# Kernel optimization log

Measured on AMD Instinct MI355X. Metric: run time of the kernel, lower is better.

## Reference

```python
import jax, jax.numpy as jnp
import numpy as np

NORM_EPS = 1e-6


def setup_inputs() -> dict:
    key = jax.random.key(0)
    k1, k2 = jax.random.split(key)
    in_features, out_features = 4096, 4096
    x = jax.random.normal(k1, (2, 2048, in_features), dtype=jnp.float32)
    scale = 1.0 / np.sqrt(in_features)
    weight = jax.random.normal(k2, (out_features, in_features), dtype=jnp.float32) * scale
    norm_weight = jnp.ones((in_features,), dtype=jnp.float32)
    return {"x": x, "weight": weight, "norm_weight": norm_weight}


def reference(x, weight, norm_weight):
    # RMSNorm over the last dim
    rms = jnp.sqrt(jnp.mean(x * x, axis=-1, keepdims=True) + NORM_EPS)
    x_n = x / rms * norm_weight
    # ternary weight quantization (absmean scale alpha)
    alpha = jnp.maximum(jnp.mean(jnp.abs(weight)), 1e-10)
    w_q = jnp.clip(jnp.round(weight / alpha), -1.0, 1.0)
    # per-token int8 activation quantization (absmax scale gamma)
    gamma = jnp.maximum(jnp.max(jnp.abs(x_n), axis=-1, keepdims=True), 1e-10)
    x_q = jnp.clip(jnp.round(x_n * 127.0 / gamma), -128.0, 127.0)
    # rescaled matmul: y = x_q @ w_q.T * (alpha * gamma / 127)
    y = jnp.einsum('bsk,nk->bsn', x_q, w_q) * (alpha * gamma / 127.0)
    return y
```

## Files before the change

### kernel.cpp

```cpp
#include <hip/hip_runtime.h>
#include <cstdint>
#include <cstddef>


#define KD 4096
#define MD 4096
#define ND 4096

#define WBLK 512

typedef int i32x4 __attribute__((ext_vector_type(4)));

__device__ __forceinline__ void gl2lds16(const signed char* g, signed char* l) {
  __builtin_amdgcn_global_load_lds(
      (const __attribute__((address_space(1))) void*)g,
      (__attribute__((address_space(3))) void*)l, 16, 0, 0);
}

__device__ __forceinline__ float wave_sum(float v) {
#pragma unroll
  for (int off = 32; off; off >>= 1) v += __shfl_down(v, off, 64);
  return v;
}
__device__ __forceinline__ float wave_max(float v) {
#pragma unroll
  for (int off = 32; off; off >>= 1) v = fmaxf(v, __shfl_down(v, off, 64));
  return v;
}


__global__ __launch_bounds__(256) void k_alpha_part(const float* __restrict__ w,
                                                    float* __restrict__ part) {
  __shared__ float red[4];
  const int tid = threadIdx.x;
  const float4* w4 = (const float4*)(w + (size_t)blockIdx.x * 4096);
  float s = 0.f;
#pragma unroll
  for (int i = 0; i < 4; ++i) {
    float4 v = w4[i * 256 + tid];
    s += fabsf(v.x) + fabsf(v.y) + fabsf(v.z) + fabsf(v.w);
  }
  s = wave_sum(s);
  if ((tid & 63) == 0) red[tid >> 6] = s;
  __syncthreads();
  if (tid == 0) part[blockIdx.x] = (red[0] + red[1]) + (red[2] + red[3]);
}


__device__ __forceinline__ uint32_t qw4(float4 v, float alpha) {
  int q0 = (int)fminf(fmaxf(rintf(v.x / alpha), -1.f), 1.f);
  int q1 = (int)fminf(fmaxf(rintf(v.y / alpha), -1.f), 1.f);
  int q2 = (int)fminf(fmaxf(rintf(v.z / alpha), -1.f), 1.f);
  int q3 = (int)fminf(fmaxf(rintf(v.w / alpha), -1.f), 1.f);
  return (uint32_t)(q0 & 255) | ((uint32_t)(q1 & 255) << 8) |
         ((uint32_t)(q2 & 255) << 16) | ((uint32_t)(q3 & 255) << 24);
}

__global__ __launch_bounds__(256) void k_quant_all(const float* __restrict__ w,
                                                   const float* __restrict__ x,
                                                   const float* __restrict__ nw,
                                                   const float* __restrict__ part,
                                                   signed char* __restrict__ wq,
                                                   signed char* __restrict__ xq,
                                                   float* __restrict__ gamma,
                                                   float* __restrict__ alpha_out) {
  const int tid = threadIdx.x;
  const int bid = blockIdx.x;
  __shared__ float red[4];
  __shared__ float red2[4];

  if (bid < 4096) {
    const int row = bid;
    const float4* x4 = (const float4*)(x + (size_t)row * 4096);
    const float4* n4 = (const float4*)nw;
    float4 xv[4], nv[4];
#pragma unroll
    for (int i = 0; i < 4; ++i) {
      xv[i] = x4[i * 256 + tid];
      nv[i] = n4[i * 256 + tid];
    }
    float ss = 0.f, mx = 0.f;
#pragma unroll
    for (int i = 0; i < 4; ++i) {
      ss += xv[i].x * xv[i].x + xv[i].y * xv[i].y + xv[i].z * xv[i].z +
            xv[i].w * xv[i].w;
      mx = fmaxf(mx,
                 fmaxf(fmaxf(fabsf(xv[i].x * nv[i].x), fabsf(xv[i].y * nv[i].y)),
                       fmaxf(fabsf(xv[i].z * nv[i].z), fabsf(xv[i].w * nv[i].w))));
    }
    ss = wave_sum(ss);
    mx = wave_max(mx);
    if ((tid & 63) == 0) {
      red[tid >> 6] = ss;
      red2[tid >> 6] = mx;
    }
    __syncthreads();
    const float tot = (red[0] + red[1]) + (red[2] + red[3]);
    const float rms = sqrtf(tot * (1.0f / 4096.0f) + 1e-6f);
    const float mxr = fmaxf(fmaxf(red2[0], red2[1]), fmaxf(red2[2], red2[3]));
    const float g = fmaxf(mxr / rms, 1e-10f);
    if (tid == 0) gamma[row] = g;
    const float inv = 127.0f / (rms * g);

    uint32_t* xqi = (uint32_t*)(xq + (size_t)row * 4096);
#pragma unroll
    for (int i = 0; i < 4; ++i) {
      const int f = i * 256 + tid;
      int q0 = (int)fminf(fmaxf(rintf(xv[i].x * nv[i].x * inv), -128.f), 127.f);
      int q1 = (int)fminf(fmaxf(rintf(xv[i].y * nv[i].y * inv), -128.f), 127.f);
      int q2 = (int)fminf(fmaxf(rintf(xv[i].z * nv[i].z * inv), -128.f), 127.f);
      int q3 = (int)fminf(fmaxf(rintf(xv[i].w * nv[i].w * inv), -128.f), 127.f);
      xqi[f] = (uint32_t)(q0 & 255) | ((uint32_t)(q1 & 255) << 8) |
               ((uint32_t)(q2 & 255) << 16) | ((uint32_t)(q3 & 255) << 24);
    }
  } else {
    const int wb = bid - 4096;
    float s = 0.f;
#pragma unroll
    for (int i = 0; i < 16; ++i) s += part[i * 256 + tid];
    s = wave_sum(s);
    if ((tid & 63) == 0) red[tid >> 6] = s;
    __syncthreads();
    const float alpha =
        fmaxf(((red[0] + red[1]) + (red[2] + red[3])) * (1.0f / 16777216.0f),
              1e-10f);
    if (wb == 0 && tid == 0) alpha_out[0] = alpha;

    const float4* w4 = (const float4*)w;
    uint32_t* wqi = (uint32_t*)wq;
#pragma unroll 1
    for (int k = 0; k < 32; k += 4) {
      const int f0 = (wb * 32 + k) * 256 + tid;
      float4 v0 = w4[f0];
      float4 v1 = w4[f0 + 256];
      float4 v2 = w4[f0 + 512];
      float4 v3 = w4[f0 + 768];
      wqi[f0] = qw4(v0, alpha);
      wqi[f0 + 256] = qw4(v1, alpha);
      wqi[f0 + 512] = qw4(v2, alpha);
      wqi[f0 + 768] = qw4(v3, alpha);
    }
  }
}


#define BM 256
#define BN 256
#define BK 64

__global__ __launch_bounds__(512, 2) void k_gemm(const signed char* __restrict__ xq,
                                                 const signed char* __restrict__ wq,
                                                 const float* __restrict__ gamma,
                                                 const float* __restrict__ alpha_p,
                                                 float* __restrict__ out) {
  __shared__ __align__(16) signed char As_[2 * 16384];
  const int tid = threadIdx.x;
  const int lane = tid & 63;
  const int wave = tid >> 6;
  const int wm = (wave >> 2) * 128;
  const int wn = (wave & 3) * 64;
  const int quad = lane >> 4;
  const int l16 = lane & 15;

  const int x = blockIdx.x & 7;
  const int r = blockIdx.x >> 3;
  const int bm = ((x & 3) * 4 + (r >> 3)) * BM;
  const int bn = ((x >> 2) * 8 + (r & 7)) * BN;

  const int lr = lane >> 2;
  const int sc = (lane & 3) ^ ((lane >> 3) & 3);
  const int rb0 = wave * 16;
  const int rb1 = (8 + wave) * 16;
  const signed char* ag0 = xq + (size_t)(bm + rb0 + lr) * KD + sc * 16;
  const signed char* ag1 = xq + (size_t)(bm + rb1 + lr) * KD + sc * 16;
  const int lA0 = rb0 * BK;
  const int lA1 = rb1 * BK;

  const int pos = (quad ^ ((l16 >> 1) & 3)) * 16;

  const signed char* bgf[4];
#pragma unroll
  for (int ni = 0; ni < 4; ++ni)
    bgf[ni] = wq + (size_t)(bn + wn + ni * 16 + l16) * KD + quad * 16;

  i32x4 acc[8][4];
#pragma unroll
  for (int i = 0; i < 8; ++i)
#pragma unroll
    for (int j = 0; j < 4; ++j) acc[i][j] = (i32x4){0, 0, 0, 0};

  i32x4 bf[4], bfn[4], af[2];

  gl2lds16(ag0, As_ + lA0);
  gl2lds16(ag1, As_ + lA1);
#pragma unroll
  for (int ni = 0; ni < 4; ++ni) bf[ni] = *(const i32x4*)bgf[ni];
  __syncthreads();

  for (int t = 0; t < 64; ++t) {
    const int c = t & 1;
    const signed char* Ab = As_ + c * 16384;
    signed char* An = As_ + (c ^ 1) * 16384;
    const size_t kn = (size_t)(t + 1) * BK;
    const bool more = (t < 63);

#pragma unroll
    for (int p = 0; p < 4; ++p) {
#pragma unroll
      for (int j = 0; j < 2; ++j)
        af[j] = *(const i32x4*)&Ab[(wm + (p * 2 + j) * 16 + l16) * BK + pos];

      if (more && p == 0) {
#pragma unroll
        for (int ni = 0; ni < 4; ++ni)
          bfn[ni] = *(const i32x4*)(bgf[ni] + kn);
        gl2lds16(ag0 + kn, An + lA0);
        gl2lds16(ag1 + kn, An + lA1);
      }
      __builtin_amdgcn_s_barrier();
      __builtin_amdgcn_s_setprio(1);
#pragma unroll
      for (int j = 0; j < 2; ++j)
#pragma unroll
        for (int ni = 0; ni < 4; ++ni)
          acc[p * 2 + j][ni] = __builtin_amdgcn_mfma_i32_16x16x64_i8(
              af[j], bf[ni], acc[p * 2 + j][ni], 0, 0, 0);
      __builtin_amdgcn_s_setprio(0);
      if (p < 3) __builtin_amdgcn_s_barrier();
    }
    __syncthreads();
    if (more) {
#pragma unroll
      for (int ni = 0; ni < 4; ++ni) bf[ni] = bfn[ni];
    }
  }

  const float alpha = alpha_p[0];
#pragma unroll
  for (int mi = 0; mi < 8; ++mi) {
#pragma unroll
    for (int r2 = 0; r2 < 4; ++r2) {
      const int m = bm + wm + mi * 16 + quad * 4 + r2;
      const float s = (alpha * gamma[m]) / 127.0f;
#pragma unroll
      for (int ni = 0; ni < 4; ++ni) {
        const int n = bn + wn + ni * 16 + l16;
        out[(size_t)m * ND + n] = (float)acc[mi][ni][r2] * s;
      }
    }
  }
}


extern "C" void kernel_launch(void* const* d_in, const int* in_sizes, int n_in,
                              void* d_out, int out_size, void* d_ws, size_t ws_size,
                              hipStream_t stream) {
  const float* x = (const float*)d_in[0];
  const float* w = (const float*)d_in[1];
  const float* nw = (const float*)d_in[2];
  float* out = (float*)d_out;

  char* ws = (char*)d_ws;
  signed char* xq = (signed char*)ws;
  signed char* wq = (signed char*)(ws + ((size_t)1 << 24));
  float* gamma = (float*)(ws + ((size_t)2 << 24));
  float* part = (float*)(ws + ((size_t)2 << 24) + 16384);
  float* alpha = (float*)(ws + ((size_t)2 << 24) + 32768);

  k_alpha_part<<<4096, 256, 0, stream>>>(w, part);
  k_quant_all<<<4096 + WBLK, 256, 0, stream>>>(w, x, nw, part, wq, xq, gamma, alpha);
  k_gemm<<<dim3(256), dim3(512), 0, stream>>>(xq, wq, gamma, alpha, out);
}
```

Measured before the change: 262.5 us.

## Triple-buffer A tiles in LDS with prefetch two tiles ahead

Moves the A-operand LDS staging from double to triple buffering, so global-to-LDS loads are issued two K-tiles ahead. The end-of-tile __syncthreads becomes a partial vmcnt wait plus a barrier. The loop is unrolled by two to ping-pong B register fragments and avoid the register copy. This is meant to hide global load latency better. It raises LDS use to 48KB per block, which may reduce occupancy with two blocks per CU, and it relies on hand-tuned waitcnt counts being correct.

```diff
diff --git a/kernel.cpp b/kernel.cpp
--- a/kernel.cpp
+++ b/kernel.cpp
@@ -153,7 +153,7 @@
                                                  const float* __restrict__ gamma,
                                                  const float* __restrict__ alpha_p,
                                                  float* __restrict__ out) {
-  __shared__ __align__(16) signed char As_[2 * 16384];
+  __shared__ __align__(16) signed char As_[3 * 16384];
   const int tid = threadIdx.x;
   const int lane = tid & 63;
   const int wave = tid >> 6;
@@ -189,51 +189,60 @@
 #pragma unroll
     for (int j = 0; j < 4; ++j) acc[i][j] = (i32x4){0, 0, 0, 0};
 
-  i32x4 bf[4], bfn[4], af[2];
+  i32x4 bfA[4], bfB[4];
 
   gl2lds16(ag0, As_ + lA0);
   gl2lds16(ag1, As_ + lA1);
 #pragma unroll
-  for (int ni = 0; ni < 4; ++ni) bf[ni] = *(const i32x4*)bgf[ni];
+  for (int ni = 0; ni < 4; ++ni) bfA[ni] = *(const i32x4*)bgf[ni];
+  gl2lds16(ag0 + BK, As_ + 16384 + lA0);
+  gl2lds16(ag1 + BK, As_ + 16384 + lA1);
   __syncthreads();
 
-  for (int t = 0; t < 64; ++t) {
-    const int c = t & 1;
-    const signed char* Ab = As_ + c * 16384;
-    signed char* An = As_ + (c ^ 1) * 16384;
-    const size_t kn = (size_t)(t + 1) * BK;
-    const bool more = (t < 63);
-
-#pragma unroll
-    for (int p = 0; p < 4; ++p) {
-#pragma unroll
-      for (int j = 0; j < 2; ++j)
-        af[j] = *(const i32x4*)&Ab[(wm + (p * 2 + j) * 16 + l16) * BK + pos];
-
-      if (more && p == 0) {
-#pragma unroll
-        for (int ni = 0; ni < 4; ++ni)
-          bfn[ni] = *(const i32x4*)(bgf[ni] + kn);
-        gl2lds16(ag0 + kn, An + lA0);
-        gl2lds16(ag1 + kn, An + lA1);
-      }
-      __builtin_amdgcn_s_barrier();
-      __builtin_amdgcn_s_setprio(1);
-#pragma unroll
-      for (int j = 0; j < 2; ++j)
-#pragma unroll
-        for (int ni = 0; ni < 4; ++ni)
-          acc[p * 2 + j][ni] = __builtin_amdgcn_mfma_i32_16x16x64_i8(
-              af[j], bf[ni], acc[p * 2 + j][ni], 0, 0, 0);
-      __builtin_amdgcn_s_setprio(0);
-      if (p < 3) __builtin_amdgcn_s_barrier();
-    }
-    __syncthreads();
-    if (more) {
-#pragma unroll
-      for (int ni = 0; ni < 4; ++ni) bf[ni] = bfn[ni];
-    }
-  }
+  int cb = 0;
+
+#define TILE_BODY(T_, BFC, BFN)                                                \
+  {                                                                            \
+    const signed char* Ab = As_ + cb * 16384;                                  \
+    const int sb = (cb == 0) ? 2 : cb - 1;                                     \
+    signed char* An = As_ + sb * 16384;                                        \
+    i32x4 af[2];                                                               \
+    _Pragma("unroll") for (int p = 0; p < 4; ++p) {                            \
+      _Pragma("unroll") for (int j = 0; j < 2; ++j) af[j] =                    \
+          *(const i32x4*)&Ab[(wm + (p * 2 + j) * 16 + l16) * BK + pos];        \
+      if (p == 0 && (T_) < 63) {                                               \
+        _Pragma("unroll") for (int ni = 0; ni < 4; ++ni) BFN[ni] =             \
+            *(const i32x4*)(bgf[ni] + (size_t)((T_) + 1) * BK);                \
+      } else if (p == 1 && (T_) < 62) {                                        \
+        gl2lds16(ag0 + (size_t)((T_) + 2) * BK, An + lA0);                     \
+        gl2lds16(ag1 + (size_t)((T_) + 2) * BK, An + lA1);                     \
+      }                                                                        \
+      __builtin_amdgcn_s_barrier();                                            \
+      __builtin_amdgcn_s_setprio(1);                                           \
+      _Pragma("unroll") for (int j = 0; j < 2; ++j)                            \
+          _Pragma("unroll") for (int ni = 0; ni < 4; ++ni) acc[p * 2 + j][ni] =\
+              __builtin_amdgcn_mfma_i32_16x16x64_i8(af[j], BFC[ni],            \
+                                                    acc[p * 2 + j][ni], 0, 0,  \
+                                                    0);                        \
+      __builtin_amdgcn_s_setprio(0);                                           \
+      if (p < 3) __builtin_amdgcn_s_barrier();                                 \
+    }                                                                          \
+    if ((T_) < 62) {                                                           \
+      asm volatile("s_waitcnt vmcnt(2)" ::: "memory");                         \
+      __builtin_amdgcn_s_barrier();                                            \
+    } else if ((T_) == 62) {                                                   \
+      asm volatile("s_waitcnt vmcnt(0)" ::: "memory");                         \
+      __builtin_amdgcn_s_barrier();                                            \
+    }                                                                          \
+    cb = (cb == 2) ? 0 : cb + 1;                                               \
+  }
+
+  for (int t2 = 0; t2 < 32; ++t2) {
+    const int te = 2 * t2;
+    TILE_BODY(te, bfA, bfB);
+    TILE_BODY(te + 1, bfB, bfA);
+  }
+#undef TILE_BODY
 
   const float alpha = alpha_p[0];
 #pragma unroll
```

After: 265.9 us. No clear change (+1.3%).
